# Performance work log

Hardware: AMD Instinct MI355X
Metric: run time of the kernel (lower is better)

## Reference

```python
import jax, jax.numpy as jnp
import numpy as np

B, S, H = 2, 2048, 2048
NH = 16
HD = H // NH  # 128


def setup_inputs() -> dict:
    key = jax.random.key(0)
    ks = jax.random.split(key, 10)
    std = 0.02
    hidden_states = jax.random.normal(ks[0], (B, S, H), dtype=jnp.float32)
    # causal additive mask, broadcastable to [B, NH, S, S]
    causal = jnp.tril(jnp.ones((S, S), dtype=jnp.float32))
    attention_mask = jnp.where(causal == 1, 0.0, -1e9)[None, None, :, :] * jnp.ones((B, 1, 1, 1), jnp.float32)
    Wq = jax.random.normal(ks[1], (H, H), jnp.float32) * std
    Wk = jax.random.normal(ks[2], (H, H), jnp.float32) * std
    Wv = jax.random.normal(ks[3], (H, H), jnp.float32) * std
    Wo = jax.random.normal(ks[4], (H, H), jnp.float32) * std
    bq = jnp.zeros((H,), jnp.float32)
    bk = jnp.zeros((H,), jnp.float32)
    bv = jnp.zeros((H,), jnp.float32)
    bo = jnp.zeros((H,), jnp.float32)
    return {"hidden_states": hidden_states, "attention_mask": attention_mask,
            "Wq": Wq, "bq": bq, "Wk": Wk, "bk": bk, "Wv": Wv, "bv": bv, "Wo": Wo, "bo": bo}


def reference(hidden_states, attention_mask, Wq, bq, Wk, bk, Wv, bv, Wo, bo):
    b, s, _ = hidden_states.shape
    q = (hidden_states @ Wq + bq).reshape(b, s, NH, HD)
    k = (hidden_states @ Wk + bk).reshape(b, s, NH, HD)
    v = (hidden_states @ Wv + bv).reshape(b, s, NH, HD)
    # [b, h, s_q, s_k]
    scores = jnp.einsum('bqhd,bkhd->bhqk', q, k) / jnp.sqrt(jnp.float32(HD))
    scores = scores + attention_mask
    probs = jax.nn.softmax(scores, axis=-1)
    out = jnp.einsum('bhqk,bkhd->bqhd', probs, v).reshape(b, s, H)
    return out @ Wo + bo
```

## Files before the change

kernel.cpp:

```cpp
#include <hip/hip_runtime.h>
#include <hip/hip_bf16.h>
#include <stdint.h>

#define SEQ 2048
#define HID 2048
#define NHEAD 16
#define HDIM 128

typedef __attribute__((ext_vector_type(8))) short short8;
typedef __attribute__((ext_vector_type(4))) float f32x4;

__device__ __forceinline__ short f2bf(float f) {
  union { float f; unsigned u; } x; x.f = f;
  unsigned r = (x.u + 0x7FFFu + ((x.u >> 16) & 1u)) >> 16;
  return (short)r;
}

__device__ __forceinline__ void async_ld16(const void* g, void* l) {
  __builtin_amdgcn_global_load_lds(
      (__attribute__((address_space(1))) void*)g,
      (__attribute__((address_space(3))) void*)l, 16, 0, 0);
}

__global__ __launch_bounds__(256) void k_convert(const float* __restrict__ X,
                                                 short* __restrict__ Xb) {
  int i = blockIdx.x * 256 + threadIdx.x;
  float4 v = ((const float4*)X)[i];
  short4 o;
  o.x = f2bf(v.x); o.y = f2bf(v.y); o.z = f2bf(v.z); o.w = f2bf(v.w);
  ((short4*)Xb)[i] = o;
}

__global__ __launch_bounds__(256) void k_transpose(const float* __restrict__ W0,
                                                   const float* __restrict__ W1,
                                                   const float* __restrict__ W2,
                                                   const float* __restrict__ W3,
                                                   short* __restrict__ Wt) {
  __shared__ float t[32][33];
  int z = blockIdx.z;
  const float* W = (z == 0) ? W0 : (z == 1) ? W1 : (z == 2) ? W2 : W3;
  short* o = Wt + (size_t)z * HID * HID;
  int k0 = blockIdx.x * 32, n0 = blockIdx.y * 32;
  int tx = threadIdx.x, ty = threadIdx.y;
  for (int i = 0; i < 4; ++i) {
    int r = ty + i * 8;
    t[r][tx] = W[(size_t)(k0 + r) * HID + n0 + tx];
  }
  __syncthreads();
  for (int i = 0; i < 4; ++i) {
    int r = ty + i * 8;
    o[(size_t)(n0 + r) * HID + k0 + tx] = f2bf(t[tx][r]);
  }
}

__global__ __launch_bounds__(256) void k_gemm_qkv(const short* __restrict__ A,
                                                  const short* __restrict__ Bt,
                                                  const float* __restrict__ bqp,
                                                  const float* __restrict__ bkp,
                                                  const float* __restrict__ bvp,
                                                  short* __restrict__ Qb,
                                                  short* __restrict__ Kb,
                                                  short* __restrict__ VtG) {
  __shared__ short smem[128 * 136];
  short* As = smem;
  short* Bs = smem + 128 * 32;
  const int tid = threadIdx.x;
  const int wave = tid >> 6, lane = tid & 63;
  const int col = lane & 15, quad = lane >> 4;
  const int wm = wave >> 1, wn = wave & 1;
  const int m0 = blockIdx.y * 128;
  const int n0g = blockIdx.x * 128;
  const int j = n0g >> 11;
  const int n0 = n0g & 2047;
  const int K = HID;
  const float* bias = (j == 0) ? bqp : (j == 1) ? bkp : bvp;

  f32x4 acc[4][4];
  for (int i = 0; i < 4; ++i)
    for (int jj = 0; jj < 4; ++jj)
      acc[i][jj] = (f32x4){0.f, 0.f, 0.f, 0.f};

  for (int k0 = 0; k0 < K; k0 += 32) {
    __syncthreads();
    for (int i = 0; i < 2; ++i) {
      int c = i * 256 + tid;
      int row = c >> 2, cc = c & 3;
      async_ld16(A + (size_t)(m0 + row) * K + k0 + cc * 8,
                 (char*)As + (i * 256 + wave * 64) * 16);
      async_ld16(Bt + (size_t)(n0g + row) * K + k0 + cc * 8,
                 (char*)Bs + (i * 256 + wave * 64) * 16);
    }
    __syncthreads();
    short8 af[4], bf[4];
    for (int mi = 0; mi < 4; ++mi)
      af[mi] = *(const short8*)(As + (wm * 64 + mi * 16 + col) * 32 + quad * 8);
    for (int ni = 0; ni < 4; ++ni)
      bf[ni] = *(const short8*)(Bs + (wn * 64 + ni * 16 + col) * 32 + quad * 8);
    for (int mi = 0; mi < 4; ++mi)
      for (int ni = 0; ni < 4; ++ni)
        acc[mi][ni] =
            __builtin_amdgcn_mfma_f32_16x16x32_bf16(af[mi], bf[ni], acc[mi][ni], 0, 0, 0);
  }

  if (j == 2) {
    __syncthreads();
    short* T = smem;
    for (int ni = 0; ni < 4; ++ni) {
      int n = wn * 64 + ni * 16 + col;
      float bv = bias[n0 + n];
      for (int mi = 0; mi < 4; ++mi)
        for (int r = 0; r < 4; ++r) {
          int m = wm * 64 + mi * 16 + quad * 4 + r;
          T[n * 136 + m] = f2bf(acc[mi][ni][r] + bv);
        }
    }
    __syncthreads();
    int h = n0 >> 7;
    int b = m0 >> 11, s0l = m0 & 2047;
    int rr = tid >> 1, halfc = tid & 1;
    short* o = VtG + ((size_t)(b * NHEAD + h) * HDIM + rr) * SEQ + s0l;
    for (int i = 0; i < 8; ++i) {
      int chunk = halfc * 8 + i;
      short8 v = *(const short8*)(T + rr * 136 + chunk * 8);
      *(short8*)(o + chunk * 8) = v;
    }
    return;
  }

  short* out = (j == 0) ? Qb : Kb;
  for (int ni = 0; ni < 4; ++ni) {
    int n = n0 + wn * 64 + ni * 16 + col;
    float bv = bias[n];
    int h = n >> 7, d = n & 127;
    for (int mi = 0; mi < 4; ++mi) {
      for (int r = 0; r < 4; ++r) {
        int m = m0 + wm * 64 + mi * 16 + quad * 4 + r;
        int b = m >> 11, s = m & 2047;
        out[((size_t)(b * NHEAD + h) * SEQ + s) * HDIM + d] = f2bf(acc[mi][ni][r] + bv);
      }
    }
  }
}

__global__ __launch_bounds__(256) void k_gemm_o(const short* __restrict__ A,
                                                const short* __restrict__ Bt,
                                                const float* __restrict__ bias,
                                                float* __restrict__ out) {
  __shared__ short As[128 * 32];
  __shared__ short Bs[128 * 32];
  const int tid = threadIdx.x;
  const int wave = tid >> 6, lane = tid & 63;
  const int col = lane & 15, quad = lane >> 4;
  const int wm = wave >> 1, wn = wave & 1;
  const int m0 = blockIdx.y * 128, n0 = blockIdx.x * 128;
  const int K = HID;

  f32x4 acc[4][4];
  for (int i = 0; i < 4; ++i)
    for (int jj = 0; jj < 4; ++jj)
      acc[i][jj] = (f32x4){0.f, 0.f, 0.f, 0.f};

  for (int k0 = 0; k0 < K; k0 += 32) {
    __syncthreads();
    for (int i = 0; i < 2; ++i) {
      int c = i * 256 + tid;
      int row = c >> 2, cc = c & 3;
      async_ld16(A + (size_t)(m0 + row) * K + k0 + cc * 8,
                 (char*)As + (i * 256 + wave * 64) * 16);
      async_ld16(Bt + (size_t)(n0 + row) * K + k0 + cc * 8,
                 (char*)Bs + (i * 256 + wave * 64) * 16);
    }
    __syncthreads();
    short8 af[4], bf[4];
    for (int mi = 0; mi < 4; ++mi)
      af[mi] = *(const short8*)(As + (wm * 64 + mi * 16 + col) * 32 + quad * 8);
    for (int ni = 0; ni < 4; ++ni)
      bf[ni] = *(const short8*)(Bs + (wn * 64 + ni * 16 + col) * 32 + quad * 8);
    for (int mi = 0; mi < 4; ++mi)
      for (int ni = 0; ni < 4; ++ni)
        acc[mi][ni] =
            __builtin_amdgcn_mfma_f32_16x16x32_bf16(af[mi], bf[ni], acc[mi][ni], 0, 0, 0);
  }

  for (int ni = 0; ni < 4; ++ni) {
    int n = n0 + wn * 64 + ni * 16 + col;
    float bv = bias[n];
    for (int mi = 0; mi < 4; ++mi)
      for (int r = 0; r < 4; ++r) {
        int m = m0 + wm * 64 + mi * 16 + quad * 4 + r;
        out[(size_t)m * HID + n] = acc[mi][ni][r] + bv;
      }
  }
}

__global__ __launch_bounds__(256) void k_attn(const short* __restrict__ Qb,
                                              const short* __restrict__ Kb,
                                              const short* __restrict__ VtG,
                                              short* __restrict__ AO) {
  __shared__ short Ks[2][64 * 128];
  __shared__ short Vt[2][128 * 64];
  __shared__ short Pb[4 * 32 * 72];

  const int bx = blockIdx.x;
  const int p = bx & 7;
  const int h = (bx >> 3) & 15;
  const int b = bx >> 7;
  const int tid = threadIdx.x;
  const int wave = tid >> 6, lane = tid & 63;
  const int col = lane & 15, quad = lane >> 4;

  const size_t ho = (size_t)(b * NHEAD + h) * SEQ * HDIM;
  const short* Qh = Qb + ho;
  const short* Kh = Kb + ho;
  const short* Vh = VtG + ho;

  const float scale = 0.08838834764831845f;
  short8 ones;
  for (int i = 0; i < 8; ++i) ones[i] = (short)0x3F80;

  const int cK = wave * 64 + lane;
  const int rowK = cK >> 4, c16 = cK & 15;
  const int srcK = c16 ^ (rowK & 7);
  const int rowV = cK >> 3, c8 = cK & 7;
  const int srcV = c8 ^ (rowV & 7);
  short* Pw = Pb + wave * 32 * 72;

  for (int which = 0; which < 2; ++which) {
    const int qb = which ? p : 15 - p;
    const int q0 = qb * 128 + wave * 32;
    const int nt = 2 * qb + 2;

    short8 qf[2][4];
    for (int m = 0; m < 2; ++m)
      for (int f = 0; f < 4; ++f)
        qf[m][f] = *(const short8*)(Qh + (size_t)(q0 + m * 16 + col) * HDIM + f * 32 + quad * 8);

    f32x4 o[2][8], osum[2];
    for (int m = 0; m < 2; ++m) {
      for (int t = 0; t < 8; ++t) o[m][t] = (f32x4){0.f, 0.f, 0.f, 0.f};
      osum[m] = (f32x4){0.f, 0.f, 0.f, 0.f};
    }

    __syncthreads();
    {
      const short* kbase = Kh + (size_t)rowK * HDIM + srcK * 8;
      const short* vbase = Vh + (size_t)rowV * SEQ + srcV * 8;
      for (int i = 0; i < 4; ++i) {
        async_ld16(kbase + (size_t)(i * 16) * HDIM, (char*)Ks[0] + (i * 256 + cK) * 16);
        async_ld16(vbase + (size_t)(i * 32) * SEQ, (char*)Vt[0] + (i * 256 + cK) * 16);
      }
    }

    for (int kb = 0; kb < nt; ++kb) {
      __syncthreads();
      const int cur = kb & 1;
      if (kb + 1 < nt) {
        const short* kbase = Kh + (size_t)((kb + 1) * 64 + rowK) * HDIM + srcK * 8;
        const short* vbase = Vh + (size_t)rowV * SEQ + (kb + 1) * 64 + srcV * 8;
        for (int i = 0; i < 4; ++i) {
          async_ld16(kbase + (size_t)(i * 16) * HDIM, (char*)Ks[cur ^ 1] + (i * 256 + cK) * 16);
          async_ld16(vbase + (size_t)(i * 32) * SEQ, (char*)Vt[cur ^ 1] + (i * 256 + cK) * 16);
        }
      }
      const short* KsC = Ks[cur];
      const short* VtC = Vt[cur];

      f32x4 s[2][4];
      for (int m = 0; m < 2; ++m)
        for (int nf = 0; nf < 4; ++nf) s[m][nf] = (f32x4){0.f, 0.f, 0.f, 0.f};
      for (int f = 0; f < 4; ++f)
        for (int nf = 0; nf < 4; ++nf) {
          short8 kf = *(const short8*)(KsC + (nf * 16 + col) * 128 +
                                       (((f * 4 + quad) ^ (col & 7)) * 8));
          s[0][nf] = __builtin_amdgcn_mfma_f32_16x16x32_bf16(qf[0][f], kf, s[0][nf], 0, 0, 0);
          s[1][nf] = __builtin_amdgcn_mfma_f32_16x16x32_bf16(qf[1][f], kf, s[1][nf], 0, 0, 0);
        }

      const bool diag = (kb >= 2 * qb);
      for (int m = 0; m < 2; ++m)
        for (int nf = 0; nf < 4; ++nf)
          for (int r = 0; r < 4; ++r) {
            float e = __expf(s[m][nf][r] * scale - 8.0f);
            if (diag) {
              int key = kb * 64 + nf * 16 + col;
              int q = q0 + m * 16 + quad * 4 + r;
              if (key > q) e = 0.f;
            }
            Pw[(m * 16 + quad * 4 + r) * 72 + nf * 16 + col] = f2bf(e);
          }

      for (int kk = 0; kk < 2; ++kk) {
        short8 pa0 = *(const short8*)(Pw + (0 * 16 + col) * 72 + kk * 32 + quad * 8);
        short8 pa1 = *(const short8*)(Pw + (1 * 16 + col) * 72 + kk * 32 + quad * 8);
        osum[0] = __builtin_amdgcn_mfma_f32_16x16x32_bf16(pa0, ones, osum[0], 0, 0, 0);
        osum[1] = __builtin_amdgcn_mfma_f32_16x16x32_bf16(pa1, ones, osum[1], 0, 0, 0);
        for (int t = 0; t < 8; ++t) {
          short8 vf = *(const short8*)(VtC + (t * 16 + col) * 64 +
                                       (((kk * 4 + quad) ^ (col & 7)) * 8));
          o[0][t] = __builtin_amdgcn_mfma_f32_16x16x32_bf16(pa0, vf, o[0][t], 0, 0, 0);
          o[1][t] = __builtin_amdgcn_mfma_f32_16x16x32_bf16(pa1, vf, o[1][t], 0, 0, 0);
        }
      }
    }

    for (int m = 0; m < 2; ++m)
      for (int r = 0; r < 4; ++r) {
        float inv = 1.f / osum[m][r];
        int q = q0 + m * 16 + quad * 4 + r;
        for (int t = 0; t < 8; ++t)
          AO[((size_t)(b * SEQ + q)) * HID + h * HDIM + 16 * t + col] = f2bf(o[m][t][r] * inv);
      }
  }
}

extern "C" void kernel_launch(void* const* d_in, const int* in_sizes, int n_in,
                              void* d_out, int out_size, void* d_ws, size_t ws_size,
                              hipStream_t stream) {
  const float* X  = (const float*)d_in[0];
  const float* Wq = (const float*)d_in[2];
  const float* bq = (const float*)d_in[3];
  const float* Wk = (const float*)d_in[4];
  const float* bk = (const float*)d_in[5];
  const float* Wv = (const float*)d_in[6];
  const float* bv = (const float*)d_in[7];
  const float* Wo = (const float*)d_in[8];
  const float* bo = (const float*)d_in[9];

  char* ws = (char*)d_ws;
  short* Xb  = (short*)(ws);
  short* Wt  = (short*)(ws + (16ull << 20));
  short* Qb  = (short*)(ws + (48ull << 20));
  short* Kb  = (short*)(ws + (64ull << 20));
  short* VtG = (short*)(ws + (80ull << 20));
  short* AO  = (short*)(ws + (96ull << 20));

  short* Wto = Wt + (size_t)3 * HID * HID;

  k_convert<<<8192, 256, 0, stream>>>(X, Xb);
  k_transpose<<<dim3(64, 64, 4), dim3(32, 8), 0, stream>>>(Wq, Wk, Wv, Wo, Wt);

  k_gemm_qkv<<<dim3(48, 32), 256, 0, stream>>>(Xb, Wt, bq, bk, bv, Qb, Kb, VtG);

  k_attn<<<2 * NHEAD * 8, 256, 0, stream>>>(Qb, Kb, VtG, AO);

  k_gemm_o<<<dim3(16, 32), 256, 0, stream>>>(AO, Wto, bo, (float*)d_out);
}
```

Measured before the change: 433.6 us.

## Run attention with 1024-thread blocks sharing K/V tiles and coalesce Q/K stores

The attention kernel now launches 16 waves per block. Eight waves handle the heavy query block and eight handle the paired light one, with each wave owning 16 query rows instead of two rows processed one after the other. All waves share one K/V double-buffered stream, so each tile is loaded once for both query blocks, and waves on the short block skip compute once past their range while still hitting the barriers. Separately, the Q/K GEMM epilogue stages results through LDS so the global writes are 16-byte coalesced. In exchange, the larger block must fit its register budget, and the waves that finish early sit idle.

```diff
diff --git a/kernel.cpp b/kernel.cpp
--- a/kernel.cpp
+++ b/kernel.cpp
@@ -102,9 +102,9 @@
             __builtin_amdgcn_mfma_f32_16x16x32_bf16(af[mi], bf[ni], acc[mi][ni], 0, 0, 0);
   }
 
+  __syncthreads();
+  short* T = smem;
   if (j == 2) {
-    __syncthreads();
-    short* T = smem;
     for (int ni = 0; ni < 4; ++ni) {
       int n = wn * 64 + ni * 16 + col;
       float bv = bias[n0 + n];
@@ -127,18 +127,25 @@
     return;
   }
 
+  for (int ni = 0; ni < 4; ++ni) {
+    int n = wn * 64 + ni * 16 + col;
+    float bv = bias[n0 + n];
+    for (int mi = 0; mi < 4; ++mi)
+      for (int r = 0; r < 4; ++r) {
+        int m = wm * 64 + mi * 16 + quad * 4 + r;
+        T[m * 136 + n] = f2bf(acc[mi][ni][r] + bv);
+      }
+  }
+  __syncthreads();
   short* out = (j == 0) ? Qb : Kb;
-  for (int ni = 0; ni < 4; ++ni) {
-    int n = n0 + wn * 64 + ni * 16 + col;
-    float bv = bias[n];
-    int h = n >> 7, d = n & 127;
-    for (int mi = 0; mi < 4; ++mi) {
-      for (int r = 0; r < 4; ++r) {
-        int m = m0 + wm * 64 + mi * 16 + quad * 4 + r;
-        int b = m >> 11, s = m & 2047;
-        out[((size_t)(b * NHEAD + h) * SEQ + s) * HDIM + d] = f2bf(acc[mi][ni][r] + bv);
-      }
-    }
+  int h = n0 >> 7;
+  for (int i = 0; i < 8; ++i) {
+    int c = i * 256 + tid;
+    int m = c >> 4, ch = c & 15;
+    int mm = m0 + m;
+    int b = mm >> 11, s = mm & 2047;
+    short8 v = *(const short8*)(T + m * 136 + ch * 8);
+    *(short8*)(out + ((size_t)(b * NHEAD + h) * SEQ + s) * HDIM + ch * 8) = v;
   }
 }
 
@@ -193,13 +200,13 @@
   }
 }
 
-__global__ __launch_bounds__(256) void k_attn(const short* __restrict__ Qb,
-                                              const short* __restrict__ Kb,
-                                              const short* __restrict__ VtG,
-                                              short* __restrict__ AO) {
+__global__ __launch_bounds__(1024) void k_attn(const short* __restrict__ Qb,
+                                               const short* __restrict__ Kb,
+                                               const short* __restrict__ VtG,
+                                               short* __restrict__ AO) {
   __shared__ short Ks[2][64 * 128];
   __shared__ short Vt[2][128 * 64];
-  __shared__ short Pb[4 * 32 * 72];
+  __shared__ short Pb[16 * 16 * 72];
 
   const int bx = blockIdx.x;
   const int p = bx & 7;
@@ -209,6 +216,13 @@
   const int wave = tid >> 6, lane = tid & 63;
   const int col = lane & 15, quad = lane >> 4;
 
+  const bool hiw = wave < 8;
+  const int wslot = wave & 7;
+  const int qb = hiw ? (15 - p) : p;
+  const int q0 = qb * 128 + wslot * 16;
+  const int nt_w = 2 * qb + 2;
+  const int nt = 2 * (15 - p) + 2;
+
   const size_t ho = (size_t)(b * NHEAD + h) * SEQ * HDIM;
   const short* Qh = Qb + ho;
   const short* Kh = Kb + ho;
@@ -218,98 +232,74 @@
   short8 ones;
   for (int i = 0; i < 8; ++i) ones[i] = (short)0x3F80;
 
-  const int cK = wave * 64 + lane;
-  const int rowK = cK >> 4, c16 = cK & 15;
+  const int rowK = tid >> 4, c16 = tid & 15;
   const int srcK = c16 ^ (rowK & 7);
-  const int rowV = cK >> 3, c8 = cK & 7;
+  const int rowV = tid >> 3, c8 = tid & 7;
   const int srcV = c8 ^ (rowV & 7);
-  short* Pw = Pb + wave * 32 * 72;
-
-  for (int which = 0; which < 2; ++which) {
-    const int qb = which ? p : 15 - p;
-    const int q0 = qb * 128 + wave * 32;
-    const int nt = 2 * qb + 2;
-
-    short8 qf[2][4];
-    for (int m = 0; m < 2; ++m)
-      for (int f = 0; f < 4; ++f)
-        qf[m][f] = *(const short8*)(Qh + (size_t)(q0 + m * 16 + col) * HDIM + f * 32 + quad * 8);
-
-    f32x4 o[2][8], osum[2];
-    for (int m = 0; m < 2; ++m) {
-      for (int t = 0; t < 8; ++t) o[m][t] = (f32x4){0.f, 0.f, 0.f, 0.f};
-      osum[m] = (f32x4){0.f, 0.f, 0.f, 0.f};
-    }
-
-    __syncthreads();
-    {
-      const short* kbase = Kh + (size_t)rowK * HDIM + srcK * 8;
-      const short* vbase = Vh + (size_t)rowV * SEQ + srcV * 8;
-      for (int i = 0; i < 4; ++i) {
-        async_ld16(kbase + (size_t)(i * 16) * HDIM, (char*)Ks[0] + (i * 256 + cK) * 16);
-        async_ld16(vbase + (size_t)(i * 32) * SEQ, (char*)Vt[0] + (i * 256 + cK) * 16);
-      }
-    }
-
-    for (int kb = 0; kb < nt; ++kb) {
-      __syncthreads();
-      const int cur = kb & 1;
-      if (kb + 1 < nt) {
-        const short* kbase = Kh + (size_t)((kb + 1) * 64 + rowK) * HDIM + srcK * 8;
-        const short* vbase = Vh + (size_t)rowV * SEQ + (kb + 1) * 64 + srcV * 8;
-        for (int i = 0; i < 4; ++i) {
-          async_ld16(kbase + (size_t)(i * 16) * HDIM, (char*)Ks[cur ^ 1] + (i * 256 + cK) * 16);
-          async_ld16(vbase + (size_t)(i * 32) * SEQ, (char*)Vt[cur ^ 1] + (i * 256 + cK) * 16);
+  short* Pw = Pb + wave * 16 * 72;
+
+  short8 qf[4];
+  for (int f = 0; f < 4; ++f)
+    qf[f] = *(const short8*)(Qh + (size_t)(q0 + col) * HDIM + f * 32 + quad * 8);
+
+  f32x4 o[8], osum;
+  for (int t = 0; t < 8; ++t) o[t] = (f32x4){0.f, 0.f, 0.f, 0.f};
+  osum = (f32x4){0.f, 0.f, 0.f, 0.f};
+
+  async_ld16(Kh + (size_t)rowK * HDIM + srcK * 8, (char*)Ks[0] + tid * 16);
+  async_ld16(Vh + (size_t)rowV * SEQ + srcV * 8, (char*)Vt[0] + tid * 16);
+
+  for (int kb = 0; kb < nt; ++kb) {
+    __syncthreads();
+    const int cur = kb & 1;
+    if (kb + 1 < nt) {
+      async_ld16(Kh + (size_t)((kb + 1) * 64 + rowK) * HDIM + srcK * 8,
+                 (char*)Ks[cur ^ 1] + tid * 16);
+      async_ld16(Vh + (size_t)rowV * SEQ + (kb + 1) * 64 + srcV * 8,
+                 (char*)Vt[cur ^ 1] + tid * 16);
+    }
+    if (kb >= nt_w) continue;
+
+    const short* KsC = Ks[cur];
+    const short* VtC = Vt[cur];
+
+    f32x4 s[4];
+    for (int nf = 0; nf < 4; ++nf) s[nf] = (f32x4){0.f, 0.f, 0.f, 0.f};
+    for (int f = 0; f < 4; ++f)
+      for (int nf = 0; nf < 4; ++nf) {
+        short8 kf = *(const short8*)(KsC + (nf * 16 + col) * 128 +
+                                     (((f * 4 + quad) ^ (col & 7)) * 8));
+        s[nf] = __builtin_amdgcn_mfma_f32_16x16x32_bf16(qf[f], kf, s[nf], 0, 0, 0);
+      }
+
+    const bool diag = (kb >= 2 * qb);
+    for (int nf = 0; nf < 4; ++nf)
+      for (int r = 0; r < 4; ++r) {
+        float e = __expf(s[nf][r] * scale - 8.0f);
+        if (diag) {
+          int key = kb * 64 + nf * 16 + col;
+          int q = q0 + quad * 4 + r;
+          if (key > q) e = 0.f;
         }
-      }
-      const short* KsC = Ks[cur];
-      const short* VtC = Vt[cur];
-
-      f32x4 s[2][4];
-      for (int m = 0; m < 2; ++m)
-        for (int nf = 0; nf < 4; ++nf) s[m][nf] = (f32x4){0.f, 0.f, 0.f, 0.f};
-      for (int f = 0; f < 4; ++f)
-        for (int nf = 0; nf < 4; ++nf) {
-          short8 kf = *(const short8*)(KsC + (nf * 16 + col) * 128 +
-                                       (((f * 4 + quad) ^ (col & 7)) * 8));
-          s[0][nf] = __builtin_amdgcn_mfma_f32_16x16x32_bf16(qf[0][f], kf, s[0][nf], 0, 0, 0);
-          s[1][nf] = __builtin_amdgcn_mfma_f32_16x16x32_bf16(qf[1][f], kf, s[1][nf], 0, 0, 0);
-        }
-
-      const bool diag = (kb >= 2 * qb);
-      for (int m = 0; m < 2; ++m)
-        for (int nf = 0; nf < 4; ++nf)
-          for (int r = 0; r < 4; ++r) {
-            float e = __expf(s[m][nf][r] * scale - 8.0f);
-            if (diag) {
-              int key = kb * 64 + nf * 16 + col;
-              int q = q0 + m * 16 + quad * 4 + r;
-              if (key > q) e = 0.f;
-            }
-            Pw[(m * 16 + quad * 4 + r) * 72 + nf * 16 + col] = f2bf(e);
-          }
-
-      for (int kk = 0; kk < 2; ++kk) {
-        short8 pa0 = *(const short8*)(Pw + (0 * 16 + col) * 72 + kk * 32 + quad * 8);
-        short8 pa1 = *(const short8*)(Pw + (1 * 16 + col) * 72 + kk * 32 + quad * 8);
-        osum[0] = __builtin_amdgcn_mfma_f32_16x16x32_bf16(pa0, ones, osum[0], 0, 0, 0);
-        osum[1] = __builtin_amdgcn_mfma_f32_16x16x32_bf16(pa1, ones, osum[1], 0, 0, 0);
-        for (int t = 0; t < 8; ++t) {
-          short8 vf = *(const short8*)(VtC + (t * 16 + col) * 64 +
-                                       (((kk * 4 + quad) ^ (col & 7)) * 8));
-          o[0][t] = __builtin_amdgcn_mfma_f32_16x16x32_bf16(pa0, vf, o[0][t], 0, 0, 0);
-          o[1][t] = __builtin_amdgcn_mfma_f32_16x16x32_bf16(pa1, vf, o[1][t], 0, 0, 0);
-        }
-      }
-    }
-
-    for (int m = 0; m < 2; ++m)
-      for (int r = 0; r < 4; ++r) {
-        float inv = 1.f / osum[m][r];
-        int q = q0 + m * 16 + quad * 4 + r;
-        for (int t = 0; t < 8; ++t)
-          AO[((size_t)(b * SEQ + q)) * HID + h * HDIM + 16 * t + col] = f2bf(o[m][t][r] * inv);
-      }
+        Pw[(quad * 4 + r) * 72 + nf * 16 + col] = f2bf(e);
+      }
+
+    for (int kk = 0; kk < 2; ++kk) {
+      short8 pa = *(const short8*)(Pw + col * 72 + kk * 32 + quad * 8);
+      osum = __builtin_amdgcn_mfma_f32_16x16x32_bf16(pa, ones, osum, 0, 0, 0);
+      for (int t = 0; t < 8; ++t) {
+        short8 vf = *(const short8*)(VtC + (t * 16 + col) * 64 +
+                                     (((kk * 4 + quad) ^ (col & 7)) * 8));
+        o[t] = __builtin_amdgcn_mfma_f32_16x16x32_bf16(pa, vf, o[t], 0, 0, 0);
+      }
+    }
+  }
+
+  for (int r = 0; r < 4; ++r) {
+    float inv = 1.f / osum[r];
+    int q = q0 + quad * 4 + r;
+    for (int t = 0; t < 8; ++t)
+      AO[((size_t)(b * SEQ + q)) * HID + h * HDIM + 16 * t + col] = f2bf(o[t][r] * inv);
   }
 }
 
@@ -341,7 +331,7 @@
 
   k_gemm_qkv<<<dim3(48, 32), 256, 0, stream>>>(Xb, Wt, bq, bk, bv, Qb, Kb, VtG);
 
-  k_attn<<<2 * NHEAD * 8, 256, 0, stream>>>(Qb, Kb, VtG, AO);
+  k_attn<<<2 * NHEAD * 8, 1024, 0, stream>>>(Qb, Kb, VtG, AO);
 
   k_gemm_o<<<dim3(16, 32), 256, 0, stream>>>(AO, Wto, bo, (float*)d_out);
 }
```

Result: faster. 424.7 us (-2.0%).
